# Optimization experiments

Measured on AMD Instinct MI355X. Metric: run time of the kernel, lower is better.

Reference implementation:

```python
import jax, jax.numpy as jnp
import numpy as np

N_NODES = 200000   # node frontier pool size per layer
N_ENT = 10000
BATCH = 256
N_LAYER = 3
N_EDGES = 1000000
REL_VOCAB = 402    # 2*n_rel + 2 with n_rel=200
HID = 20


def setup_inputs() -> dict:
    key = jax.random.key(0)
    ks = jax.random.split(key, 12)
    return {
        "query_rel": jax.random.randint(ks[0], (BATCH,), 0, REL_VOCAB, dtype=jnp.int32),
        "src_idx": jax.random.randint(ks[1], (N_LAYER, N_EDGES), 0, N_NODES, dtype=jnp.int32),
        "rel_idx": jax.random.randint(ks[2], (N_LAYER, N_EDGES), 0, REL_VOCAB, dtype=jnp.int32),
        "batch_idx": jax.random.randint(ks[3], (N_LAYER, N_EDGES), 0, BATCH, dtype=jnp.int32),
        "dst_idx": jax.random.randint(ks[4], (N_LAYER, N_EDGES), 0, N_NODES, dtype=jnp.int32),
        "final_batch": jax.random.randint(ks[5], (N_NODES,), 0, BATCH, dtype=jnp.int32),
        "final_ent": jax.random.randint(ks[6], (N_NODES,), 0, N_ENT, dtype=jnp.int32),
        "rela_embed": jax.random.normal(ks[7], (REL_VOCAB, HID), dtype=jnp.float32),
        "W1": jax.random.normal(ks[8], (30, 60), dtype=jnp.float32) * 0.1,
        "W2": jax.random.normal(ks[9], (1, 30), dtype=jnp.float32) * 0.1,
        "Wc": jax.random.normal(ks[10], (1, HID), dtype=jnp.float32) * 0.1,
        "bc": jnp.zeros((1,), dtype=jnp.float32),
    }


def reference(query_rel, src_idx, rel_idx, batch_idx, dst_idx,
              final_batch, final_ent, rela_embed, W1, W2, Wc, bc):
    q_emb_all = rela_embed[query_rel]  # [B, 20] query relation embedding per batch query

    def layer(hidden, edges):
        src, rel, bidx, dst = edges
        h_src = hidden[src]            # [E, 20] gather current node states
        r_emb = rela_embed[rel]        # [E, 20]
        q_emb = q_emb_all[bidx]        # [E, 20]
        attn_in = jnp.concatenate([h_src, r_emb, q_emb], axis=1)  # [E, 60]
        # attention MLP: sigmoid(W2 @ relu(W1 @ x)), 60 -> 30 -> 1
        score = jax.nn.sigmoid(jax.nn.relu(attn_in @ W1.T) @ W2.T)  # [E, 1]
        msg = score * (h_src + r_emb)  # [E, 20] embed_rel weighted by attention
        # sparse attention-weighted aggregation (torch.sparse.mm)
        new_hidden = jax.ops.segment_sum(msg, dst, num_segments=N_NODES)
        return new_hidden, None

    hidden0 = jnp.zeros((N_NODES, HID), dtype=rela_embed.dtype)
    hidden, _ = jax.lax.scan(layer, hidden0, (src_idx, rel_idx, batch_idx, dst_idx))

    result = (hidden @ Wc.T + bc).reshape(-1)  # [N_NODES] linear classifier
    score_all = jnp.zeros((BATCH, N_ENT), dtype=result.dtype)
    score_all = score_all.at[final_batch, final_ent].set(result)
    return score_all
```

## Files before the change

### kernel.cpp

```cpp
#include <hip/hip_runtime.h>
#include <hip/hip_bf16.h>
#include <hip/hip_fp16.h>

#define N_NODES 200000
#define N_ENT   10000
#define BATCH   256
#define N_LAYER 3
#define N_EDGES 1000000
#define REL_VOCAB 402
#define HID 20
#define CAP 32
#define HPADH 32

__global__ __launch_bounds__(256) void tables_kernel(
    const float* __restrict__ W1, const float* __restrict__ rela,
    const int* __restrict__ query_rel,
    float* __restrict__ R1T, float* __restrict__ Q1T)
{
    int t = blockIdx.x * blockDim.x + threadIdx.x;
    if (t < 30 * REL_VOCAB) {
        int j = t / REL_VOCAB, r = t % REL_VOCAB;
        const float* w  = W1 + j * 60 + 20;
        const float* re = rela + (size_t)r * HID;
        float a = 0.f;
        #pragma unroll
        for (int k = 0; k < HID; ++k) a = fmaf(w[k], re[k], a);
        R1T[t] = a;
    } else if (t < 30 * REL_VOCAB + 30 * BATCH) {
        int u = t - 30 * REL_VOCAB;
        int j = u / BATCH, b = u % BATCH;
        int qr = query_rel[b];
        const float* w  = W1 + j * 60 + 40;
        const float* qe = rela + (size_t)qr * HID;
        float a = 0.f;
        #pragma unroll
        for (int k = 0; k < HID; ++k) a = fmaf(w[k], qe[k], a);
        Q1T[j * BATCH + b] = a;
    }
}

__global__ __launch_bounds__(256) void score0_kernel(
    const float* __restrict__ R1T, const float* __restrict__ Q1T,
    const float* __restrict__ W2, float* __restrict__ score0)
{
    int t = blockIdx.x * blockDim.x + threadIdx.x;
    if (t >= BATCH * REL_VOCAB) return;
    int b = t / REL_VOCAB, r = t % REL_VOCAB;
    float hs = 0.f;
    #pragma unroll 5
    for (int j = 0; j < 30; ++j) {
        float v = R1T[j * REL_VOCAB + r] + Q1T[j * BATCH + b];
        hs = fmaf(W2[j], fmaxf(v, 0.f), hs);
    }
    score0[t] = 1.f / (1.f + __expf(-hs));
}

template<int LAYER>
__global__ __launch_bounds__(256) void msg_rec_kernel(
    const int* __restrict__ src, const int* __restrict__ rel,
    const int* __restrict__ bidx, const int* __restrict__ dst,
    const __half* __restrict__ h16,
    const float* __restrict__ W1, const float* __restrict__ W2,
    const float* __restrict__ R1T, const float* __restrict__ Q1T,
    const float* __restrict__ score0,
    int* __restrict__ cnt, unsigned long long* __restrict__ recs)
{
    int e = blockIdx.x * blockDim.x + threadIdx.x;
    if (e >= N_EDGES) return;
    const int r = __builtin_nontemporal_load(&rel[e]);
    const int b = __builtin_nontemporal_load(&bidx[e]);
    const int d = __builtin_nontemporal_load(&dst[e]);

    float score;
    unsigned int srec = 0;
    if (LAYER == 0) {
        score = score0[b * REL_VOCAB + r];
    } else {
        const int s = __builtin_nontemporal_load(&src[e]);
        srec = (unsigned int)s;
        float hv[HID];
        const uint2* hp = reinterpret_cast<const uint2*>(h16 + (size_t)s * HPADH);
        #pragma unroll
        for (int c = 0; c < 5; ++c) {
            uint2 v = hp[c];
            __half2 a0 = *reinterpret_cast<__half2*>(&v.x);
            __half2 a1 = *reinterpret_cast<__half2*>(&v.y);
            float2 f0 = __half22float2(a0), f1 = __half22float2(a1);
            hv[4*c+0] = f0.x; hv[4*c+1] = f0.y; hv[4*c+2] = f1.x; hv[4*c+3] = f1.y;
        }
        float hs = 0.f;
        #pragma unroll 3
        for (int j = 0; j < 30; ++j) {
            float t = R1T[j * REL_VOCAB + r] + Q1T[j * BATCH + b];
            const float* w = W1 + j * 60;
            #pragma unroll
            for (int k = 0; k < HID; ++k) t = fmaf(w[k], hv[k], t);
            hs = fmaf(W2[j], fmaxf(t, 0.f), hs);
        }
        score = 1.f / (1.f + __expf(-hs));
    }

    int pos = atomicAdd(&cnt[d], 1);
    if (pos < CAP) {
        __half sc = __float2half(score);
        unsigned int lo = (unsigned int)(unsigned short)r |
                          ((unsigned int)__half_as_ushort(sc) << 16);
        unsigned long long pk = (unsigned long long)srec |
                                ((unsigned long long)lo << 32);
        __builtin_nontemporal_store(pk, &recs[(size_t)d * CAP + pos]);
    }
}

template<int LAYER>
__global__ __launch_bounds__(256) void gather_rec_kernel(
    const int* __restrict__ cnt, const unsigned long long* __restrict__ recs,
    const __half* __restrict__ h16_in,
    const float* __restrict__ rela,
    __half* __restrict__ h16_out)
{
    int tid = blockIdx.x * blockDim.x + threadIdx.x;
    if (tid >= N_NODES * 5) return;
    const int d = tid / 5;
    const int c = tid % 5;
    int n = cnt[d];
    if (n > CAP) n = CAP;

    const unsigned long long* rp = recs + (size_t)d * CAP;
    float4 acc = make_float4(0.f, 0.f, 0.f, 0.f);
    for (int i = 0; i < n; ++i) {
        const unsigned long long rec = rp[i];
        const unsigned int hi = (unsigned int)(rec >> 32);
        const int r = (int)(hi & 0xFFFFu);
        const float score = __half2float(__ushort_as_half((unsigned short)(hi >> 16)));
        float4 rv = *reinterpret_cast<const float4*>(rela + (size_t)r * HID + c * 4);
        float4 m = rv;
        if (LAYER != 0) {
            const int s = (int)(unsigned int)(rec & 0xFFFFFFFFull);
            uint2 hvv = *reinterpret_cast<const uint2*>(h16_in + (size_t)s * HPADH + c * 4);
            __half2 a0 = *reinterpret_cast<__half2*>(&hvv.x);
            __half2 a1 = *reinterpret_cast<__half2*>(&hvv.y);
            float2 f0 = __half22float2(a0), f1 = __half22float2(a1);
            m.x += f0.x; m.y += f0.y; m.z += f1.x; m.w += f1.y;
        }
        acc.x = fmaf(score, m.x, acc.x);
        acc.y = fmaf(score, m.y, acc.y);
        acc.z = fmaf(score, m.z, acc.z);
        acc.w = fmaf(score, m.w, acc.w);
    }

    __half2 p0 = __floats2half2_rn(acc.x, acc.y);
    __half2 p1 = __floats2half2_rn(acc.z, acc.w);
    uint2 w = make_uint2(*reinterpret_cast<unsigned int*>(&p0),
                         *reinterpret_cast<unsigned int*>(&p1));
    *reinterpret_cast<uint2*>(h16_out + (size_t)d * HPADH + c * 4) = w;
}

__global__ __launch_bounds__(256) void gather2_kernel(
    const int* __restrict__ cnt, const unsigned long long* __restrict__ recs,
    const __half* __restrict__ h16_in,
    const float* __restrict__ rela,
    const float* __restrict__ Wc, const float* __restrict__ bc,
    float* __restrict__ val)
{
    int d = blockIdx.x * blockDim.x + threadIdx.x;
    if (d >= N_NODES) return;
    int n = cnt[d];
    if (n > CAP) n = CAP;

    float acc[HID];
    #pragma unroll
    for (int k = 0; k < HID; ++k) acc[k] = 0.f;

    const unsigned long long* rp = recs + (size_t)d * CAP;
    for (int i = 0; i < n; ++i) {
        const unsigned long long rec = rp[i];
        const unsigned int hi = (unsigned int)(rec >> 32);
        const int s = (int)(unsigned int)(rec & 0xFFFFFFFFull);
        const int r = (int)(hi & 0xFFFFu);
        const float score = __half2float(__ushort_as_half((unsigned short)(hi >> 16)));
        const float* rrow = rela + (size_t)r * HID;
        const uint2* hp = reinterpret_cast<const uint2*>(h16_in + (size_t)s * HPADH);
        #pragma unroll
        for (int c = 0; c < 5; ++c) {
            uint2 hvv = hp[c];
            __half2 a0 = *reinterpret_cast<__half2*>(&hvv.x);
            __half2 a1 = *reinterpret_cast<__half2*>(&hvv.y);
            float2 f0 = __half22float2(a0), f1 = __half22float2(a1);
            acc[4*c+0] = fmaf(score, f0.x + rrow[4*c+0], acc[4*c+0]);
            acc[4*c+1] = fmaf(score, f0.y + rrow[4*c+1], acc[4*c+1]);
            acc[4*c+2] = fmaf(score, f1.x + rrow[4*c+2], acc[4*c+2]);
            acc[4*c+3] = fmaf(score, f1.y + rrow[4*c+3], acc[4*c+3]);
        }
    }

    float v = bc[0];
    #pragma unroll
    for (int k = 0; k < HID; ++k) v = fmaf(acc[k], Wc[k], v);
    val[d] = v;
}

__global__ __launch_bounds__(256) void winner_kernel(
    const int* __restrict__ final_batch, const int* __restrict__ final_ent,
    int* __restrict__ winner)
{
    int i = blockIdx.x * blockDim.x + threadIdx.x;
    if (i >= N_NODES) return;
    const int slot = final_batch[i] * N_ENT + final_ent[i];
    atomicMax(&winner[slot], i);
}

__global__ __launch_bounds__(256) void out_kernel(
    const int* __restrict__ winner, const float* __restrict__ val,
    float* __restrict__ out)
{
    int sidx = blockIdx.x * blockDim.x + threadIdx.x;
    if (sidx >= BATCH * N_ENT) return;
    const int w = winner[sidx];
    const float v = (w >= 0) ? val[w] : 0.0f;
    __builtin_nontemporal_store(v, &out[sidx]);
}

template<bool FIRST>
__global__ __launch_bounds__(256) void edge_kernel(
    const int* __restrict__ src, const int* __restrict__ rel,
    const int* __restrict__ bidx, const int* __restrict__ dst,
    const int* __restrict__ query_rel,
    const float* __restrict__ hidden_in, float* __restrict__ hidden_out,
    const float* __restrict__ rela_embed,
    const float* __restrict__ W1, const float* __restrict__ W2)
{
    int e = blockIdx.x * blockDim.x + threadIdx.x;
    if (e >= N_EDGES) return;
    const int s = src[e];
    const int r = rel[e];
    const int b = bidx[e];
    const int d = dst[e];
    const int qr = query_rel[b];
    float x[60];
    if (FIRST) {
        #pragma unroll
        for (int k = 0; k < HID; ++k) x[k] = 0.0f;
    } else {
        const float4* hp = reinterpret_cast<const float4*>(hidden_in + (size_t)s * HID);
        #pragma unroll
        for (int k = 0; k < 5; ++k) {
            float4 v = hp[k];
            x[4*k+0] = v.x; x[4*k+1] = v.y; x[4*k+2] = v.z; x[4*k+3] = v.w;
        }
    }
    {
        const float4* rp = reinterpret_cast<const float4*>(rela_embed + (size_t)r * HID);
        #pragma unroll
        for (int k = 0; k < 5; ++k) {
            float4 v = rp[k];
            x[20+4*k+0] = v.x; x[20+4*k+1] = v.y; x[20+4*k+2] = v.z; x[20+4*k+3] = v.w;
        }
    }
    {
        const float4* qp = reinterpret_cast<const float4*>(rela_embed + (size_t)qr * HID);
        #pragma unroll
        for (int k = 0; k < 5; ++k) {
            float4 v = qp[k];
            x[40+4*k+0] = v.x; x[40+4*k+1] = v.y; x[40+4*k+2] = v.z; x[40+4*k+3] = v.w;
        }
    }
    float hsum = 0.0f;
    #pragma unroll 2
    for (int j = 0; j < 30; ++j) {
        float acc = 0.0f;
        const float* w1row = W1 + j * 60;
        #pragma unroll
        for (int k = (FIRST ? HID : 0); k < 60; ++k)
            acc = fmaf(w1row[k], x[k], acc);
        hsum = fmaf(W2[j], fmaxf(acc, 0.0f), hsum);
    }
    const float score = 1.0f / (1.0f + __expf(-hsum));
    float* outp = hidden_out + (size_t)d * HID;
    #pragma unroll
    for (int k = 0; k < HID; ++k) {
        const float m = FIRST ? (score * x[20+k]) : (score * (x[k] + x[20+k]));
        atomicAdd(outp + k, m);
    }
}

__global__ __launch_bounds__(256) void outF_kernel(
    const int* __restrict__ winner,
    const float* __restrict__ hidden,
    const float* __restrict__ Wc, const float* __restrict__ bc,
    float* __restrict__ out)
{
    int sidx = blockIdx.x * blockDim.x + threadIdx.x;
    if (sidx >= BATCH * N_ENT) return;
    const int w = winner[sidx];
    float v = 0.0f;
    if (w >= 0) {
        const float4* hp = reinterpret_cast<const float4*>(hidden + (size_t)w * HID);
        float acc = bc[0];
        #pragma unroll
        for (int k = 0; k < 5; ++k) {
            float4 h = hp[k];
            acc = fmaf(h.x, Wc[4*k+0], acc);
            acc = fmaf(h.y, Wc[4*k+1], acc);
            acc = fmaf(h.z, Wc[4*k+2], acc);
            acc = fmaf(h.w, Wc[4*k+3], acc);
        }
        v = acc;
    }
    out[sidx] = v;
}

extern "C" void kernel_launch(void* const* d_in, const int* in_sizes, int n_in,
                              void* d_out, int out_size, void* d_ws, size_t ws_size,
                              hipStream_t stream) {
    const int*   query_rel   = (const int*)  d_in[0];
    const int*   src_idx     = (const int*)  d_in[1];
    const int*   rel_idx     = (const int*)  d_in[2];
    const int*   batch_idx   = (const int*)  d_in[3];
    const int*   dst_idx     = (const int*)  d_in[4];
    const int*   final_batch = (const int*)  d_in[5];
    const int*   final_ent   = (const int*)  d_in[6];
    const float* rela_embed  = (const float*)d_in[7];
    const float* W1          = (const float*)d_in[8];
    const float* W2          = (const float*)d_in[9];
    const float* Wc          = (const float*)d_in[10];
    const float* bc          = (const float*)d_in[11];
    float* out = (float*)d_out;

    const size_t H16P_B = (size_t)N_NODES * HPADH * sizeof(__half);
    const size_t REC_B  = (size_t)N_NODES * CAP * 8;
    const size_t CNT_B  = (size_t)N_LAYER * N_NODES * sizeof(int);
    const size_t VAL_B  = ((size_t)N_NODES * sizeof(float) + 255) & ~255ull;
    const size_t R1T_B  = ((size_t)30 * REL_VOCAB * sizeof(float) + 255) & ~255ull;
    const size_t Q1T_B  = ((size_t)30 * BATCH * sizeof(float) + 255) & ~255ull;
    const size_t SC0_B  = ((size_t)BATCH * REL_VOCAB * sizeof(float) + 255) & ~255ull;
    const size_t WIN_B  = (size_t)BATCH * N_ENT * sizeof(int);

    const size_t REQ = 2*H16P_B + REC_B + CNT_B + VAL_B
                     + R1T_B + Q1T_B + SC0_B + WIN_B;

    const size_t HF_B = (size_t)N_NODES * HID * sizeof(float);

    const int EDGE_BLOCKS = (N_EDGES + 255) / 256;
    const int NODE_BLOCKS = (N_NODES + 255) / 256;
    const int GATH_BLOCKS = (N_NODES * 5 + 255) / 256;

    char* ws = (char*)d_ws;

    if (ws_size >= REQ) {
        size_t o = 0;
        __half*             h16A   = (__half*)            (ws + o); o += H16P_B;
        __half*             h16B   = (__half*)            (ws + o); o += H16P_B;
        unsigned long long* recs   = (unsigned long long*)(ws + o); o += REC_B;
        int*                cnt    = (int*)               (ws + o); o += CNT_B;
        float*              val    = (float*)             (ws + o); o += VAL_B;
        float*              R1T    = (float*)             (ws + o); o += R1T_B;
        float*              Q1T    = (float*)             (ws + o); o += Q1T_B;
        float*              score0 = (float*)             (ws + o); o += SC0_B;
        int*                winner = (int*)               (ws + o); o += WIN_B;

        tables_kernel<<<(30*REL_VOCAB + 30*BATCH + 255)/256, 256, 0, stream>>>(
            W1, rela_embed, query_rel, R1T, Q1T);
        score0_kernel<<<(BATCH*REL_VOCAB + 255)/256, 256, 0, stream>>>(
            R1T, Q1T, W2, score0);
        hipMemsetAsync(cnt, 0, CNT_B, stream);
        hipMemsetAsync(winner, 0xFF, WIN_B, stream);
        winner_kernel<<<NODE_BLOCKS, 256, 0, stream>>>(final_batch, final_ent, winner);

        msg_rec_kernel<0><<<EDGE_BLOCKS, 256, 0, stream>>>(
            src_idx, rel_idx, batch_idx, dst_idx,
            nullptr, W1, W2, R1T, Q1T, score0, cnt, recs);
        gather_rec_kernel<0><<<GATH_BLOCKS, 256, 0, stream>>>(
            cnt, recs, nullptr, rela_embed, h16A);
        msg_rec_kernel<1><<<EDGE_BLOCKS, 256, 0, stream>>>(
            src_idx + (size_t)N_EDGES, rel_idx + (size_t)N_EDGES,
            batch_idx + (size_t)N_EDGES, dst_idx + (size_t)N_EDGES,
            h16A, W1, W2, R1T, Q1T, score0, cnt + N_NODES, recs);
        gather_rec_kernel<1><<<GATH_BLOCKS, 256, 0, stream>>>(
            cnt + N_NODES, recs, h16A, rela_embed, h16B);
        msg_rec_kernel<2><<<EDGE_BLOCKS, 256, 0, stream>>>(
            src_idx + 2*(size_t)N_EDGES, rel_idx + 2*(size_t)N_EDGES,
            batch_idx + 2*(size_t)N_EDGES, dst_idx + 2*(size_t)N_EDGES,
            h16B, W1, W2, R1T, Q1T, score0, cnt + 2*N_NODES, recs);
        gather2_kernel<<<NODE_BLOCKS, 256, 0, stream>>>(
            cnt + 2*N_NODES, recs, h16B, rela_embed, Wc, bc, val);

        out_kernel<<<(BATCH * N_ENT + 255) / 256, 256, 0, stream>>>(winner, val, out);
    } else {
        float* hiddenA = (float*)(ws);
        float* hiddenB = (float*)(ws + HF_B);
        int*   winner  = (int*)  (ws + 2 * HF_B);

        hipMemsetAsync(hiddenA, 0, HF_B, stream);
        edge_kernel<true><<<EDGE_BLOCKS, 256, 0, stream>>>(
            src_idx, rel_idx, batch_idx, dst_idx,
            query_rel, nullptr, hiddenA, rela_embed, W1, W2);

        hipMemsetAsync(hiddenB, 0, HF_B, stream);
        edge_kernel<false><<<EDGE_BLOCKS, 256, 0, stream>>>(
            src_idx + (size_t)N_EDGES, rel_idx + (size_t)N_EDGES,
            batch_idx + (size_t)N_EDGES, dst_idx + (size_t)N_EDGES,
            query_rel, hiddenA, hiddenB, rela_embed, W1, W2);

        hipMemsetAsync(hiddenA, 0, HF_B, stream);
        edge_kernel<false><<<EDGE_BLOCKS, 256, 0, stream>>>(
            src_idx + 2*(size_t)N_EDGES, rel_idx + 2*(size_t)N_EDGES,
            batch_idx + 2*(size_t)N_EDGES, dst_idx + 2*(size_t)N_EDGES,
            query_rel, hiddenB, hiddenA, rela_embed, W1, W2);

        hipMemsetAsync(winner, 0xFF, (size_t)BATCH * N_ENT * sizeof(int), stream);
        winner_kernel<<<NODE_BLOCKS, 256, 0, stream>>>(final_batch, final_ent, winner);
        outF_kernel<<<(BATCH * N_ENT + 255) / 256, 256, 0, stream>>>(winner, hiddenA, Wc, bc, out);
    }
}
```

Before: 390.5 us.

## Move the final classifier into out_kernel and reuse gather_rec for last layer

Replaces the per-node gather2 kernel (one thread per node with 20 accumulators) with the 5-lane-per-node gather_rec kernel writing fp32 hidden state. The Wc dot product moves into out_kernel, so it runs only for winning slots. The atomicAdd on cnt[d] is also issued at the top of msg_rec so its latency overlaps the score computation. In exchange the last layer writes a full fp32 hidden buffer, and out_kernel does a 20-float gather per occupied slot.

```diff
diff --git a/kernel.cpp b/kernel.cpp
--- a/kernel.cpp
+++ b/kernel.cpp
@@ -67,9 +67,10 @@
 {
     int e = blockIdx.x * blockDim.x + threadIdx.x;
     if (e >= N_EDGES) return;
+    const int d = __builtin_nontemporal_load(&dst[e]);
+    const int pos = atomicAdd(&cnt[d], 1);
     const int r = __builtin_nontemporal_load(&rel[e]);
     const int b = __builtin_nontemporal_load(&bidx[e]);
-    const int d = __builtin_nontemporal_load(&dst[e]);
 
     float score;
     unsigned int srec = 0;
@@ -100,7 +101,6 @@
         score = 1.f / (1.f + __expf(-hs));
     }
 
-    int pos = atomicAdd(&cnt[d], 1);
     if (pos < CAP) {
         __half sc = __float2half(score);
         unsigned int lo = (unsigned int)(unsigned short)r |
@@ -116,7 +116,8 @@
     const int* __restrict__ cnt, const unsigned long long* __restrict__ recs,
     const __half* __restrict__ h16_in,
     const float* __restrict__ rela,
-    __half* __restrict__ h16_out)
+    __half* __restrict__ h16_out,
+    float* __restrict__ hF_out)
 {
     int tid = blockIdx.x * blockDim.x + threadIdx.x;
     if (tid >= N_NODES * 5) return;
@@ -148,55 +149,15 @@
         acc.w = fmaf(score, m.w, acc.w);
     }
 
-    __half2 p0 = __floats2half2_rn(acc.x, acc.y);
-    __half2 p1 = __floats2half2_rn(acc.z, acc.w);
-    uint2 w = make_uint2(*reinterpret_cast<unsigned int*>(&p0),
-                         *reinterpret_cast<unsigned int*>(&p1));
-    *reinterpret_cast<uint2*>(h16_out + (size_t)d * HPADH + c * 4) = w;
-}
-
-__global__ __launch_bounds__(256) void gather2_kernel(
-    const int* __restrict__ cnt, const unsigned long long* __restrict__ recs,
-    const __half* __restrict__ h16_in,
-    const float* __restrict__ rela,
-    const float* __restrict__ Wc, const float* __restrict__ bc,
-    float* __restrict__ val)
-{
-    int d = blockIdx.x * blockDim.x + threadIdx.x;
-    if (d >= N_NODES) return;
-    int n = cnt[d];
-    if (n > CAP) n = CAP;
-
-    float acc[HID];
-    #pragma unroll
-    for (int k = 0; k < HID; ++k) acc[k] = 0.f;
-
-    const unsigned long long* rp = recs + (size_t)d * CAP;
-    for (int i = 0; i < n; ++i) {
-        const unsigned long long rec = rp[i];
-        const unsigned int hi = (unsigned int)(rec >> 32);
-        const int s = (int)(unsigned int)(rec & 0xFFFFFFFFull);
-        const int r = (int)(hi & 0xFFFFu);
-        const float score = __half2float(__ushort_as_half((unsigned short)(hi >> 16)));
-        const float* rrow = rela + (size_t)r * HID;
-        const uint2* hp = reinterpret_cast<const uint2*>(h16_in + (size_t)s * HPADH);
-        #pragma unroll
-        for (int c = 0; c < 5; ++c) {
-            uint2 hvv = hp[c];
-            __half2 a0 = *reinterpret_cast<__half2*>(&hvv.x);
-            __half2 a1 = *reinterpret_cast<__half2*>(&hvv.y);
-            float2 f0 = __half22float2(a0), f1 = __half22float2(a1);
-            acc[4*c+0] = fmaf(score, f0.x + rrow[4*c+0], acc[4*c+0]);
-            acc[4*c+1] = fmaf(score, f0.y + rrow[4*c+1], acc[4*c+1]);
-            acc[4*c+2] = fmaf(score, f1.x + rrow[4*c+2], acc[4*c+2]);
-            acc[4*c+3] = fmaf(score, f1.y + rrow[4*c+3], acc[4*c+3]);
-        }
-    }
-
-    float v = bc[0];
-    #pragma unroll
-    for (int k = 0; k < HID; ++k) v = fmaf(acc[k], Wc[k], v);
-    val[d] = v;
+    if (LAYER == 2) {
+        reinterpret_cast<float4*>(hF_out)[(size_t)d * 5 + c] = acc;
+    } else {
+        __half2 p0 = __floats2half2_rn(acc.x, acc.y);
+        __half2 p1 = __floats2half2_rn(acc.z, acc.w);
+        uint2 w = make_uint2(*reinterpret_cast<unsigned int*>(&p0),
+                             *reinterpret_cast<unsigned int*>(&p1));
+        *reinterpret_cast<uint2*>(h16_out + (size_t)d * HPADH + c * 4) = w;
+    }
 }
 
 __global__ __launch_bounds__(256) void winner_kernel(
@@ -210,13 +171,28 @@
 }
 
 __global__ __launch_bounds__(256) void out_kernel(
-    const int* __restrict__ winner, const float* __restrict__ val,
+    const int* __restrict__ winner,
+    const float* __restrict__ hidden,
+    const float* __restrict__ Wc, const float* __restrict__ bc,
     float* __restrict__ out)
 {
     int sidx = blockIdx.x * blockDim.x + threadIdx.x;
     if (sidx >= BATCH * N_ENT) return;
     const int w = winner[sidx];
-    const float v = (w >= 0) ? val[w] : 0.0f;
+    float v = 0.0f;
+    if (w >= 0) {
+        const float4* hp = reinterpret_cast<const float4*>(hidden + (size_t)w * HID);
+        float acc = bc[0];
+        #pragma unroll
+        for (int k = 0; k < 5; ++k) {
+            float4 h = hp[k];
+            acc = fmaf(h.x, Wc[4*k+0], acc);
+            acc = fmaf(h.y, Wc[4*k+1], acc);
+            acc = fmaf(h.z, Wc[4*k+2], acc);
+            acc = fmaf(h.w, Wc[4*k+3], acc);
+        }
+        v = acc;
+    }
     __builtin_nontemporal_store(v, &out[sidx]);
 }
 
@@ -326,19 +302,17 @@
     const float* bc          = (const float*)d_in[11];
     float* out = (float*)d_out;
 
+    const size_t HF_B   = (size_t)N_NODES * HID * sizeof(float);
     const size_t H16P_B = (size_t)N_NODES * HPADH * sizeof(__half);
     const size_t REC_B  = (size_t)N_NODES * CAP * 8;
     const size_t CNT_B  = (size_t)N_LAYER * N_NODES * sizeof(int);
-    const size_t VAL_B  = ((size_t)N_NODES * sizeof(float) + 255) & ~255ull;
     const size_t R1T_B  = ((size_t)30 * REL_VOCAB * sizeof(float) + 255) & ~255ull;
     const size_t Q1T_B  = ((size_t)30 * BATCH * sizeof(float) + 255) & ~255ull;
     const size_t SC0_B  = ((size_t)BATCH * REL_VOCAB * sizeof(float) + 255) & ~255ull;
     const size_t WIN_B  = (size_t)BATCH * N_ENT * sizeof(int);
 
-    const size_t REQ = 2*H16P_B + REC_B + CNT_B + VAL_B
+    const size_t REQ = HF_B + 2*H16P_B + REC_B + CNT_B
                      + R1T_B + Q1T_B + SC0_B + WIN_B;
-
-    const size_t HF_B = (size_t)N_NODES * HID * sizeof(float);
 
     const int EDGE_BLOCKS = (N_EDGES + 255) / 256;
     const int NODE_BLOCKS = (N_NODES + 255) / 256;
@@ -348,11 +322,11 @@
 
     if (ws_size >= REQ) {
         size_t o = 0;
+        float*              hF     = (float*)             (ws + o); o += HF_B;
         __half*             h16A   = (__half*)            (ws + o); o += H16P_B;
         __half*             h16B   = (__half*)            (ws + o); o += H16P_B;
         unsigned long long* recs   = (unsigned long long*)(ws + o); o += REC_B;
         int*                cnt    = (int*)               (ws + o); o += CNT_B;
-        float*              val    = (float*)             (ws + o); o += VAL_B;
         float*              R1T    = (float*)             (ws + o); o += R1T_B;
         float*              Q1T    = (float*)             (ws + o); o += Q1T_B;
         float*              score0 = (float*)             (ws + o); o += SC0_B;
@@ -370,21 +344,21 @@
             src_idx, rel_idx, batch_idx, dst_idx,
             nullptr, W1, W2, R1T, Q1T, score0, cnt, recs);
         gather_rec_kernel<0><<<GATH_BLOCKS, 256, 0, stream>>>(
-            cnt, recs, nullptr, rela_embed, h16A);
+            cnt, recs, nullptr, rela_embed, h16A, nullptr);
         msg_rec_kernel<1><<<EDGE_BLOCKS, 256, 0, stream>>>(
             src_idx + (size_t)N_EDGES, rel_idx + (size_t)N_EDGES,
             batch_idx + (size_t)N_EDGES, dst_idx + (size_t)N_EDGES,
             h16A, W1, W2, R1T, Q1T, score0, cnt + N_NODES, recs);
         gather_rec_kernel<1><<<GATH_BLOCKS, 256, 0, stream>>>(
-            cnt + N_NODES, recs, h16A, rela_embed, h16B);
+            cnt + N_NODES, recs, h16A, rela_embed, h16B, nullptr);
         msg_rec_kernel<2><<<EDGE_BLOCKS, 256, 0, stream>>>(
             src_idx + 2*(size_t)N_EDGES, rel_idx + 2*(size_t)N_EDGES,
             batch_idx + 2*(size_t)N_EDGES, dst_idx + 2*(size_t)N_EDGES,
             h16B, W1, W2, R1T, Q1T, score0, cnt + 2*N_NODES, recs);
-        gather2_kernel<<<NODE_BLOCKS, 256, 0, stream>>>(
-            cnt + 2*N_NODES, recs, h16B, rela_embed, Wc, bc, val);
-
-        out_kernel<<<(BATCH * N_ENT + 255) / 256, 256, 0, stream>>>(winner, val, out);
+        gather_rec_kernel<2><<<GATH_BLOCKS, 256, 0, stream>>>(
+            cnt + 2*N_NODES, recs, h16B, rela_embed, nullptr, hF);
+
+        out_kernel<<<(BATCH * N_ENT + 255) / 256, 256, 0, stream>>>(winner, hF, Wc, bc, out);
     } else {
         float* hiddenA = (float*)(ws);
         float* hiddenB = (float*)(ws + HF_B);
```

After: 376.5 us. 1.04x faster.
